# Kernel optimization log

Hardware: AMD Instinct MI355X
Metric: run time of the kernel (lower is better)

## Reference

```python
import jax, jax.numpy as jnp
import numpy as np

DIM = 240
LATENT = 8
TRIALITY = 3
NUM_EXPERTS = 8
TOP_K = 2
DEPTH = 8
B, S = 8, 2048
EPS = 1e-5  # torch LayerNorm default


def get_e8_roots():
    roots = []
    for i in range(8):
        for j in range(i + 1, 8):
            for s0, s1 in [(1, 1), (1, -1), (-1, 1), (-1, -1)]:
                v = np.zeros(8, dtype=np.float32)
                v[i] = s0
                v[j] = s1
                roots.append(v)
                roots.append(-v)
    for signs in range(1 << 8):
        v = np.array([1 if signs & (1 << k) else -1 for k in range(8)], dtype=np.float32) * 0.5
        if bin(signs).count('1') % 2 == 0:
            roots.append(v)
            roots.append(-v)
    roots = np.stack(roots[:240]).astype(np.float32)
    return roots / np.linalg.norm(roots, axis=-1, keepdims=True)


def setup_inputs() -> dict:
    key = jax.random.key(0)
    ks = jax.random.split(key, 6)
    x = jax.random.normal(ks[0], (B, S, DIM), dtype=jnp.float32)
    roots = jnp.asarray(get_e8_roots())  # [240, 8] buffer
    proj_W = jax.random.normal(ks[1], (LATENT, DIM // TRIALITY), dtype=jnp.float32) * 0.02
    gate_W = jax.random.normal(ks[2], (DEPTH, DIM, NUM_EXPERTS), dtype=jnp.float32) * 0.02
    gate_b = jnp.zeros((DEPTH, NUM_EXPERTS), dtype=jnp.float32)
    expert_W = jax.random.normal(ks[3], (DEPTH, NUM_EXPERTS, DIM, DIM), dtype=jnp.float32) * 0.02
    expert_b = jnp.zeros((DEPTH, NUM_EXPERTS, DIM), dtype=jnp.float32)
    ln_gamma = jnp.ones((DIM,), dtype=jnp.float32)
    ln_beta = jnp.zeros((DIM,), dtype=jnp.float32)
    head_W = jax.random.normal(ks[4], (DIM, 1), dtype=jnp.float32) * 0.02
    head_b = jnp.zeros((1,), dtype=jnp.float32)
    return dict(x=x, step=10, roots=roots, proj_W=proj_W, gate_W=gate_W, gate_b=gate_b,
                expert_W=expert_W, expert_b=expert_b, ln_gamma=ln_gamma, ln_beta=ln_beta,
                head_W=head_W, head_b=head_b)


def _layernorm(h, g, b):
    m = h.mean(-1, keepdims=True)
    v = ((h - m) ** 2).mean(-1, keepdims=True)
    return (h - m) / jnp.sqrt(v + EPS) * g + b


def _cycle_block(x, step, roots, proj_W):
    s = x.shape[1]
    pos_emb = roots[jnp.arange(s) % 240]          # [S, 8]
    low_dim = pos_emb @ proj_W                     # [S, 80]
    emb = jnp.tile(low_dim, (1, TRIALITY))         # [S, 240]
    pump = 0.8 * jnp.sin(step * 0.006 * 2.0 * jnp.pi)
    x1 = x * (jnp.cos(emb) + pump)
    x2 = jnp.roll(x1, 1, axis=-1) * jnp.sin(emb)
    x3 = jnp.roll(x2, 1, axis=-1) * jnp.cos(emb)
    return (x1 + x2 + x3) / TRIALITY


def _moe_layer(h, gW, gb, eW, eb):
    gate = jax.nn.softmax(h @ gW + gb, axis=-1)               # [b,s,E]
    tw, ti = jax.lax.top_k(gate, TOP_K)                       # [b,s,k]
    tw = tw / tw.sum(-1, keepdims=True)
    # per-expert combine weight (0 for non-selected experts)
    combine = (jax.nn.one_hot(ti, NUM_EXPERTS, dtype=h.dtype) * tw[..., None]).sum(-2)  # [b,s,E]
    eout = jnp.einsum('bsd,edf->bsef', h, eW) + eb            # [b,s,E,f]
    return jnp.einsum('bsef,bse->bsf', eout, combine)


def reference(x, step, roots, proj_W, gate_W, gate_b, expert_W, expert_b,
              ln_gamma, ln_beta, head_W, head_b):
    h = _cycle_block(x, step, roots, proj_W)

    def body(h, p):
        gW, gb, eW, eb = p
        h = _moe_layer(h, gW, gb, eW, eb)
        h = h + _layernorm(h, ln_gamma, ln_beta)  # norm of layer output, as in source
        return h, None

    h, _ = jax.lax.scan(body, h, (gate_W, gate_b, expert_W, expert_b))
    pooled = h.mean(axis=1)                       # [b, dim]
    return jax.nn.sigmoid(pooled @ head_W + head_b)
```

## Files before the change

kernel.cpp:

```cpp
#include <hip/hip_runtime.h>
#include <math.h>

#define DIM 240
#define NE 8
#define DEPTH 8
#define BB 8
#define SS 2048
#define NTOK (BB * SS)
#define TWO_PI 6.28318530717958647692f
#define NPAIR 28
#define PCAP 4096
#define ASS 264
#define MT 64
#define CMT 32
#define LTILES (PCAP / MT)

typedef __attribute__((ext_vector_type(8))) short s16x8;
typedef __attribute__((ext_vector_type(4))) float f32x4;

#define ALIGN256(x) (((x) + 255) & ~((size_t)255))
static constexpr size_t HBSZ   = (size_t)NPAIR * PCAP * DIM * 2;
static constexpr size_t ENTSZ  = (size_t)NPAIR * PCAP * 4;
static constexpr size_t OFF_HB0    = 0;
static constexpr size_t OFF_HB1    = ALIGN256(OFF_HB0 + HBSZ);
static constexpr size_t OFF_ET0    = ALIGN256(OFF_HB1 + HBSZ);
static constexpr size_t OFF_ET1    = ALIGN256(OFF_ET0 + ENTSZ);
static constexpr size_t OFF_WL0    = ALIGN256(OFF_ET1 + ENTSZ);
static constexpr size_t OFF_WL1    = ALIGN256(OFF_WL0 + ENTSZ);
static constexpr size_t OFF_WH0    = ALIGN256(OFF_WL1 + ENTSZ);
static constexpr size_t OFF_WH1    = ALIGN256(OFF_WH0 + ENTSZ);
static constexpr size_t OFF_CUR    = ALIGN256(OFF_WH1 + ENTSZ);
static constexpr size_t OFF_OUTACC = ALIGN256(OFF_CUR + DEPTH*NPAIR*4);
static constexpr size_t WPACK_PER_E = 8 * 16 * 64 * 8;
static constexpr size_t OFF_WPACK  = ALIGN256(OFF_OUTACC + 8*4);
static constexpr size_t OFF_GWP    = ALIGN256(OFF_WPACK + 64*WPACK_PER_E*2);

__device__ inline short f2bf(float x) {
    unsigned u = __builtin_bit_cast(unsigned, x);
    u += 0x7fffu + ((u >> 16) & 1u);
    return (short)(u >> 16);
}
__device__ inline float bf2f(short s) {
    unsigned u = ((unsigned)(unsigned short)s) << 16;
    return __builtin_bit_cast(float, u);
}
__device__ inline int pidx(int a, int b) {
    return a*7 - ((a*(a-1)) >> 1) + (b - a - 1);
}

struct GAux {
    float lg[MT][NE];
    int   le[MT], lli[MT], lpos[MT];
    float lwl[MT], lwh[MT];
    int   lcnt[NPAIR], lbase[NPAIR];
};

__device__ void pair_gate(const short* hsb, GAux* X, const int* stok,
                          int NT, int ntok, const short* gWp,
                          int* __restrict__ cursor_out,
                          int* __restrict__ entT, float* __restrict__ wlo,
                          float* __restrict__ whi, short* __restrict__ hbo, int tid) {
    int wave = tid >> 6, lane = tid & 63;
    if (tid < NPAIR) X->lcnt[tid] = 0;
    if (wave * 16 < NT) {
        f32x4 g = (f32x4){0.f, 0.f, 0.f, 0.f};
        const short* ar = hsb + (wave*16 + (lane & 15))*ASS + (lane >> 4)*8;
#pragma unroll
        for (int ks = 0; ks < 8; ++ks) {
            s16x8 af = *(const s16x8*)(ar + ks*32);
            s16x8 bf = *(const s16x8*)(gWp + ks*512 + lane*8);
            g = __builtin_amdgcn_mfma_f32_16x16x32_bf16(af, bf, g, 0, 0, 0);
        }
        int e = lane & 15;
        if (e < NE) {
            int r0 = wave*16 + (lane >> 4)*4;
            X->lg[r0+0][e] = g[0];
            X->lg[r0+1][e] = g[1];
            X->lg[r0+2][e] = g[2];
            X->lg[r0+3][e] = g[3];
        }
    }
    __syncthreads();
    if (tid < ntok) {
        int i0 = 0; float v0 = X->lg[tid][0];
#pragma unroll
        for (int k = 1; k < NE; ++k) { float v = X->lg[tid][k]; if (v > v0) { v0 = v; i0 = k; } }
        int i1 = -1; float v1 = -1e30f;
#pragma unroll
        for (int k = 0; k < NE; ++k) { float v = X->lg[tid][k]; if (k != i0 && v > v1) { v1 = v; i1 = k; } }
        float e1 = expf(v1 - v0);
        float w0 = 1.0f / (1.0f + e1);
        float w1 = e1 / (1.0f + e1);
        int a = min(i0, i1), b = max(i0, i1);
        X->lwl[tid] = (i0 < i1) ? w0 : w1;
        X->lwh[tid] = (i0 < i1) ? w1 : w0;
        int c = pidx(a, b);
        int li = atomicAdd(&X->lcnt[c], 1);
        X->le[tid] = c; X->lli[tid] = li;
    }
    __syncthreads();
    if (tid < NPAIR && X->lcnt[tid] > 0)
        X->lbase[tid] = atomicAdd(&cursor_out[tid], X->lcnt[tid]);
    __syncthreads();
    if (tid < ntok) {
        int c = X->le[tid];
        int pos = c*PCAP + X->lbase[c] + X->lli[tid];
        X->lpos[tid] = pos;
        entT[pos] = stok[tid];
        wlo[pos]  = X->lwl[tid];
        whi[pos]  = X->lwh[tid];
    }
    __syncthreads();
    for (int idx = tid; idx < ntok*30; idx += 256) {
        int row = idx / 30, c8 = idx - row*30;
        *(s16x8*)(hbo + (size_t)X->lpos[row]*DIM + c8*8) =
            *(const s16x8*)(hsb + row*ASS + c8*8);
    }
}


__global__ __launch_bounds__(256) void k_cycle(
        const float* __restrict__ x, const int* __restrict__ step,
        const float* __restrict__ roots, const float* __restrict__ projW,
        const float* __restrict__ gateW, const float* __restrict__ eW,
        int* __restrict__ cursor0, int* __restrict__ entT0,
        float* __restrict__ wlo0, float* __restrict__ whi0, short* __restrict__ hb0,
        short* __restrict__ gwp, short* __restrict__ wp) {
    int bid = blockIdx.x, tid = threadIdx.x;
    int wave = tid >> 6, lane = tid & 63;

    if (bid >= 2560) {
        int L = bid - 2560;
        for (int ks = wave; ks < 8; ks += 4) {
            int e = lane & 15;
            int d0 = ks*32 + (lane >> 4)*8;
            short v[8];
#pragma unroll
            for (int j = 0; j < 8; ++j) {
                int d = d0 + j;
                v[j] = (e < NE && d < DIM) ? f2bf(gateW[(size_t)L*DIM*NE + d*NE + e]) : (short)0;
            }
            *(s16x8*)(gwp + ((size_t)L*8 + ks)*512 + lane*8) = *(s16x8*)v;
        }
        return;
    }
    if (bid >= 512) {
        int unit = (bid - 512)*4 + wave;
        int eg = unit >> 7;
        int rem = unit & 127;
        int ks = rem >> 4, tile = rem & 15;
        int f  = tile*16 + (lane & 15);
        int d0 = ks*32 + (lane >> 4)*8;
        const float* W = eW + (size_t)eg*DIM*DIM;
        short v[8];
#pragma unroll
        for (int j = 0; j < 8; ++j) {
            int d = d0 + j;
            v[j] = (d < DIM && f < DIM) ? f2bf(W[(size_t)d*DIM + f]) : (short)0;
        }
        *(s16x8*)(wp + (((size_t)eg*8 + ks)*16 + tile)*512 + lane*8) = *(s16x8*)v;
        return;
    }

    __shared__ short hsb[CMT*ASS];
    __shared__ GAux X;
    __shared__ int stok[CMT];
    __shared__ short gwl[8*512];
    __shared__ float pjw[8*80];

    int tok0 = bid * CMT;
    if (tid < CMT) stok[tid] = tok0 + tid;
    for (int idx = tid; idx < CMT*12; idx += 256) {
        int row = idx / 12, c = 240 + (idx - row*12)*2;
        *(int*)(hsb + row*ASS + c) = 0;
    }
    for (int i = tid; i < 8*80; i += 256) pjw[i] = projW[i];
    for (int u = tid; u < 512; u += 256) {
        int ks = u >> 6, l64 = u & 63;
        int e = l64 & 15, d0 = ks*32 + (l64 >> 4)*8;
        short v[8];
#pragma unroll
        for (int j = 0; j < 8; ++j) {
            int d = d0 + j;
            v[j] = (e < NE && d < DIM) ? f2bf(gateW[d*NE + e]) : (short)0;
        }
        *(s16x8*)(gwl + u*8) = *(s16x8*)v;
    }
    __syncthreads();

    float pump = 0.8f * sinf((float)step[0] * 0.006f * TWO_PI);
    if (lane < 60) {
        int d0 = lane * 4;
        for (int jt = 0; jt < 8; ++jt) {
            int lt = wave * 8 + jt;
            int tok = tok0 + lt;
            int smr = (tok & (SS-1)) % 240;
            const float* xr = x + (size_t)tok * DIM;
            float r8[8];
#pragma unroll
            for (int r = 0; r < 8; ++r) r8[r] = roots[smr*8 + r];
            float xv[6], c6[6], s6[6];
#pragma unroll
            for (int j = 0; j < 6; ++j) {
                int d = d0 - 2 + j; if (d < 0) d += DIM;
                int jm = d % 80;
                float acc = 0.f;
#pragma unroll
                for (int r = 0; r < 8; ++r) acc += r8[r] * pjw[r*80 + jm];
                c6[j] = cosf(acc); s6[j] = sinf(acc);
                xv[j] = xr[d];
            }
            float x1[6];
#pragma unroll
            for (int j = 0; j < 6; ++j) x1[j] = xv[j] * (c6[j] + pump);
            short ob[4];
#pragma unroll
            for (int k = 0; k < 4; ++k)
                ob[k] = f2bf((x1[k+2] + x1[k+1]*s6[k+2] + x1[k]*s6[k+1]*c6[k+2]) * (1.0f/3.0f));
            *(short4*)(hsb + lt*ASS + d0) = *(short4*)ob;
        }
    }
    __syncthreads();
    pair_gate(hsb, &X, stok, CMT, CMT, gwl, cursor0, entT0, wlo0, whi0, hb0, tid);
}

__global__ __launch_bounds__(256, 2) void k_layer(
        const short* __restrict__ hb_in, const int* __restrict__ entT_in,
        const float* __restrict__ wlo_in, const float* __restrict__ whi_in,
        short* __restrict__ hb_out, int* __restrict__ entT_out,
        float* __restrict__ wlo_out, float* __restrict__ whi_out,
        const short* __restrict__ wpack, const float* __restrict__ eb,
        const float* __restrict__ gamma, const float* __restrict__ beta,
        const short* __restrict__ gwp_next,
        const int* __restrict__ cursor_in, int* __restrict__ cursor_out,
        const float* __restrict__ headW, float* __restrict__ out_acc,
        int l, int do_gate) {
    __shared__ short As[MT*ASS];
    __shared__ GAux X;
    __shared__ float swl[MT], swh[MT];
    __shared__ int stok[MT];
    __shared__ float part[4][MT][2];
    __shared__ float mrs[MT][2];
    __shared__ float pool[BB];

    int p = blockIdx.x, tile = blockIdx.y;
    int cnt = cursor_in[p];
    int t0 = tile * MT;
    if (t0 >= cnt) return;
    int ntok = min(MT, cnt - t0);
    int tid = threadIdx.x, wave = tid >> 6, lane = tid & 63;
    int a = 0, rem = p;
    while (rem >= 7 - a) { rem -= 7 - a; ++a; }
    int b = a + 1 + rem;
    size_t base = (size_t)p * PCAP + t0;

    if (tid < MT) {
        if (tid < ntok) { stok[tid] = entT_in[base+tid]; swl[tid] = wlo_in[base+tid]; swh[tid] = whi_in[base+tid]; }
        else            { stok[tid] = 0; swl[tid] = 0.f; swh[tid] = 0.f; }
    }
    if (tid < BB) pool[tid] = 0.f;
#pragma unroll
    for (int it = 0; it < 8; ++it) {
        int idx = tid + it * 256;
        int row = idx >> 5, c8 = idx & 31;
        s16x8 z = (s16x8){0,0,0,0,0,0,0,0};
        if (c8 < 30 && row < ntok)
            z = *(const s16x8*)(hb_in + (base + row)*DIM + c8*8);
        *(s16x8*)(As + row*ASS + ((c8 < 30) ? c8*8 : (240 + (c8-30)*8))) = z;
    }
    __syncthreads();

    f32x4 accA[4][4], accB[4][4];
#pragma unroll
    for (int m = 0; m < 4; ++m)
#pragma unroll
        for (int n = 0; n < 4; ++n) { accA[m][n] = (f32x4){0,0,0,0}; accB[m][n] = (f32x4){0,0,0,0}; }

    const short* ab = As + (lane & 15)*ASS + (lane >> 4)*8;
    const short* wA = wpack + ((size_t)(l*NE + a))*WPACK_PER_E + (size_t)wave*4*512 + lane*8;
    const short* wB = wpack + ((size_t)(l*NE + b))*WPACK_PER_E + (size_t)wave*4*512 + lane*8;

    for (int ks = 0; ks < 8; ++ks) {
        s16x8 a0 = *(const s16x8*)(ab + ks*32 + 0*16*ASS);
        s16x8 a1 = *(const s16x8*)(ab + ks*32 + 1*16*ASS);
        s16x8 a2 = *(const s16x8*)(ab + ks*32 + 2*16*ASS);
        s16x8 a3 = *(const s16x8*)(ab + ks*32 + 3*16*ASS);
#pragma unroll
        for (int n = 0; n < 4; ++n) {
            s16x8 bA = *(const s16x8*)(wA + ((size_t)ks*16 + n)*512);
            s16x8 bB = *(const s16x8*)(wB + ((size_t)ks*16 + n)*512);
            accA[0][n] = __builtin_amdgcn_mfma_f32_16x16x32_bf16(a0, bA, accA[0][n], 0, 0, 0);
            accA[1][n] = __builtin_amdgcn_mfma_f32_16x16x32_bf16(a1, bA, accA[1][n], 0, 0, 0);
            accA[2][n] = __builtin_amdgcn_mfma_f32_16x16x32_bf16(a2, bA, accA[2][n], 0, 0, 0);
            accA[3][n] = __builtin_amdgcn_mfma_f32_16x16x32_bf16(a3, bA, accA[3][n], 0, 0, 0);
            accB[0][n] = __builtin_amdgcn_mfma_f32_16x16x32_bf16(a0, bB, accB[0][n], 0, 0, 0);
            accB[1][n] = __builtin_amdgcn_mfma_f32_16x16x32_bf16(a1, bB, accB[1][n], 0, 0, 0);
            accB[2][n] = __builtin_amdgcn_mfma_f32_16x16x32_bf16(a2, bB, accB[2][n], 0, 0, 0);
            accB[3][n] = __builtin_amdgcn_mfma_f32_16x16x32_bf16(a3, bB, accB[3][n], 0, 0, 0);
        }
    }
    __syncthreads();

    const float* ebA = eb + ((size_t)(l*NE + a))*DIM;
    const float* ebB = eb + ((size_t)(l*NE + b))*DIM;
    float bA[4], bBv[4], gg[4], bt[4]; int colv[4];
#pragma unroll
    for (int n = 0; n < 4; ++n) {
        int col = wave*64 + n*16 + (lane & 15);
        bool valid = (col < DIM);
        colv[n] = valid ? col : -1;
        bA[n]  = valid ? ebA[col]   : 0.f;
        bBv[n] = valid ? ebB[col]   : 0.f;
        gg[n]  = valid ? gamma[col] : 0.f;
        bt[n]  = valid ? beta[col]  : 0.f;
    }

#pragma unroll
    for (int m = 0; m < 4; ++m) {
#pragma unroll
        for (int r = 0; r < 4; ++r) {
            int row = m*16 + ((lane >> 4) << 2) + r;
            float wa = swl[row], wb = swh[row];
            float s = 0.f, q = 0.f;
#pragma unroll
            for (int n = 0; n < 4; ++n) {
                float y = (colv[n] >= 0)
                        ? wa*(accA[m][n][r] + bA[n]) + wb*(accB[m][n][r] + bBv[n]) : 0.f;
                s += y; q += y*y;
            }
#pragma unroll
            for (int o = 1; o <= 8; o <<= 1) {
                s += __shfl_xor(s, o, 64);
                q += __shfl_xor(q, o, 64);
            }
            if ((lane & 15) == 0) { part[wave][row][0] = s; part[wave][row][1] = q; }
        }
    }
    __syncthreads();
    if (tid < MT) {
        float s = part[0][tid][0] + part[1][tid][0] + part[2][tid][0] + part[3][tid][0];
        float q = part[0][tid][1] + part[1][tid][1] + part[2][tid][1] + part[3][tid][1];
        float mean = s * (1.0f/DIM);
        float var = q * (1.0f/DIM) - mean*mean;
        mrs[tid][0] = mean;
        mrs[tid][1] = rsqrtf(var + 1e-5f);
    }
    __syncthreads();
    for (int idx = tid; idx < MT*12; idx += 256) {
        int row = idx / 12, c = 240 + (idx - row*12)*2;
        *(int*)(As + row*ASS + c) = 0;
    }
#pragma unroll
    for (int m = 0; m < 4; ++m) {
#pragma unroll
        for (int r = 0; r < 4; ++r) {
            int row = m*16 + ((lane >> 4) << 2) + r;
            float wa = swl[row], wb = swh[row];
            float mean = mrs[row][0], rs = mrs[row][1];
#pragma unroll
            for (int n = 0; n < 4; ++n) {
                if (colv[n] >= 0) {
                    float y = wa*(accA[m][n][r] + bA[n]) + wb*(accB[m][n][r] + bBv[n]);
                    As[row*ASS + colv[n]] = f2bf(y + (y - mean)*rs*gg[n] + bt[n]);
                }
            }
        }
    }
    __syncthreads();

    if (do_gate) {
        pair_gate(As, &X, stok, MT, ntok, gwp_next,
                  cursor_out, entT_out, wlo_out, whi_out, hb_out, tid);
    } else {
        float hwv[4];
#pragma unroll
        for (int jj = 0; jj < 4; ++jj) {
            int d = lane + 64*jj;
            hwv[jj] = (d < DIM) ? headW[d] : 0.f;
        }
        for (int j = 0; j < 16; ++j) {
            int row = wave*16 + j;
            if (row >= ntok) continue;
            float ph = 0.f;
#pragma unroll
            for (int jj = 0; jj < 4; ++jj) {
                int d = lane + 64*jj;
                if (d < DIM) ph += bf2f(As[row*ASS + d]) * hwv[jj];
            }
#pragma unroll
            for (int o = 32; o > 0; o >>= 1) ph += __shfl_xor(ph, o, 64);
            if (lane == 0) atomicAdd(&pool[stok[row] / SS], ph);
        }
        __syncthreads();
        if (tid < BB) atomicAdd(&out_acc[tid], pool[tid]);
    }
}

__global__ void k_final(const float* __restrict__ out_acc, const float* __restrict__ headb,
                        float* __restrict__ out) {
    int b = threadIdx.x;
    if (b < BB) {
        float z = out_acc[b] * (1.0f/SS) + headb[0];
        out[b] = 1.0f / (1.0f + expf(-z));
    }
}

extern "C" void kernel_launch(void* const* d_in, const int* in_sizes, int n_in,
                              void* d_out, int out_size, void* d_ws, size_t ws_size,
                              hipStream_t stream) {
    (void)in_sizes; (void)n_in; (void)out_size; (void)ws_size;
    const float* x     = (const float*)d_in[0];
    const int*   step  = (const int*)  d_in[1];
    const float* roots = (const float*)d_in[2];
    const float* projW = (const float*)d_in[3];
    const float* gateW = (const float*)d_in[4];
    const float* eW    = (const float*)d_in[6];
    const float* eb    = (const float*)d_in[7];
    const float* gamma = (const float*)d_in[8];
    const float* beta  = (const float*)d_in[9];
    const float* headW = (const float*)d_in[10];
    const float* headb = (const float*)d_in[11];
    float* out = (float*)d_out;

    char* w = (char*)d_ws;
    short* hb[2]   = { (short*)(w + OFF_HB0), (short*)(w + OFF_HB1) };
    int*   et[2]   = { (int*)  (w + OFF_ET0), (int*)  (w + OFF_ET1) };
    float* wl[2]   = { (float*)(w + OFF_WL0), (float*)(w + OFF_WL1) };
    float* wh[2]   = { (float*)(w + OFF_WH0), (float*)(w + OFF_WH1) };
    int*   cursor  = (int*)  (w + OFF_CUR);
    float* out_acc = (float*)(w + OFF_OUTACC);
    short* wpack   = (short*)(w + OFF_WPACK);
    short* gwp     = (short*)(w + OFF_GWP);

    hipMemsetAsync(w + OFF_CUR, 0, (OFF_OUTACC - OFF_CUR) + BB*sizeof(float), stream);

    k_cycle<<<2568, 256, 0, stream>>>(x, step, roots, projW, gateW, eW,
                                      cursor, et[0], wl[0], wh[0], hb[0], gwp, wpack);

    for (int l = 0; l < DEPTH; ++l) {
        int in = l & 1, outp = in ^ 1;
        int do_gate = (l < DEPTH - 1);
        const short* gwn = gwp + (size_t)(do_gate ? (l+1) : 0) * 8 * 512;
        int* cur_out = cursor + (do_gate ? (l+1) : 0) * NPAIR;
        k_layer<<<dim3(NPAIR, LTILES), 256, 0, stream>>>(
            hb[in], et[in], wl[in], wh[in],
            hb[outp], et[outp], wl[outp], wh[outp],
            wpack, eb, gamma, beta, gwn,
            cursor + l*NPAIR, cur_out, headW, out_acc, l, do_gate);
    }

    k_final<<<1, 64, 0, stream>>>(out_acc, headb, out);
}
```

Baseline: 319.7 us.

## Fuse all MoE layers into one persistent per-token-tile kernel

Replaces the per-layer pair-bucketed dispatch, with its global scatter of hidden states and atomic cursors, by one kernel in which each 512-thread block keeps 64 tokens resident in LDS across all 8 layers. Inside each layer the block gates, groups its tokens by expert locally, runs the MFMA expert GEMMs on gathered rows and accumulates the weighted outputs into an fp32 LDS buffer before LayerNorm. This removes 8 launches and the global round-trips of activations. In exchange it uses roughly 120 KB of LDS, so only one block fits per CU. Expert tiles are often partly filled, which wastes MFMA work, and expert weights are re-read from L2 by every block.

New measurement: 518.0 us. 62.1% more time.

```diff
diff --git a/kernel.cpp b/kernel.cpp
--- a/kernel.cpp
+++ b/kernel.cpp
@@ -8,32 +8,34 @@
 #define SS 2048
 #define NTOK (BB * SS)
 #define TWO_PI 6.28318530717958647692f
-#define NPAIR 28
-#define PCAP 4096
 #define ASS 264
-#define MT 64
-#define CMT 32
-#define LTILES (PCAP / MT)
+#define YSS 244
+#define TPB 512
+#define ROWS 64
+#define NBLK (NTOK / ROWS)
+#define NT_TILES 15
 
 typedef __attribute__((ext_vector_type(8))) short s16x8;
 typedef __attribute__((ext_vector_type(4))) float f32x4;
 
-#define ALIGN256(x) (((x) + 255) & ~((size_t)255))
-static constexpr size_t HBSZ   = (size_t)NPAIR * PCAP * DIM * 2;
-static constexpr size_t ENTSZ  = (size_t)NPAIR * PCAP * 4;
-static constexpr size_t OFF_HB0    = 0;
-static constexpr size_t OFF_HB1    = ALIGN256(OFF_HB0 + HBSZ);
-static constexpr size_t OFF_ET0    = ALIGN256(OFF_HB1 + HBSZ);
-static constexpr size_t OFF_ET1    = ALIGN256(OFF_ET0 + ENTSZ);
-static constexpr size_t OFF_WL0    = ALIGN256(OFF_ET1 + ENTSZ);
-static constexpr size_t OFF_WL1    = ALIGN256(OFF_WL0 + ENTSZ);
-static constexpr size_t OFF_WH0    = ALIGN256(OFF_WL1 + ENTSZ);
-static constexpr size_t OFF_WH1    = ALIGN256(OFF_WH0 + ENTSZ);
-static constexpr size_t OFF_CUR    = ALIGN256(OFF_WH1 + ENTSZ);
-static constexpr size_t OFF_OUTACC = ALIGN256(OFF_CUR + DEPTH*NPAIR*4);
 static constexpr size_t WPACK_PER_E = 8 * 16 * 64 * 8;
-static constexpr size_t OFF_WPACK  = ALIGN256(OFF_OUTACC + 8*4);
-static constexpr size_t OFF_GWP    = ALIGN256(OFF_WPACK + 64*WPACK_PER_E*2);
+static constexpr size_t OFF_OUTACC = 0;
+static constexpr size_t OFF_WPACK  = 256;
+static constexpr size_t OFF_GWP    = OFF_WPACK + 64 * WPACK_PER_E * 2;
+
+#define L_HSB   0
+#define L_Y     33792
+#define L_GWL   96256
+#define L_EBL   104448
+#define L_GML   112128
+#define L_BTL   113088
+#define L_LG    114048
+#define L_RL    116096
+#define L_RW    117120
+#define L_CNT   119168
+#define L_POOL  119232
+#define L_PJW   119264
+#define SMEM_SZ 121824
 
 __device__ inline short f2bf(float x) {
     unsigned u = __builtin_bit_cast(unsigned, x);
@@ -44,93 +46,15 @@
     unsigned u = ((unsigned)(unsigned short)s) << 16;
     return __builtin_bit_cast(float, u);
 }
-__device__ inline int pidx(int a, int b) {
-    return a*7 - ((a*(a-1)) >> 1) + (b - a - 1);
-}
-
-struct GAux {
-    float lg[MT][NE];
-    int   le[MT], lli[MT], lpos[MT];
-    float lwl[MT], lwh[MT];
-    int   lcnt[NPAIR], lbase[NPAIR];
-};
-
-__device__ void pair_gate(const short* hsb, GAux* X, const int* stok,
-                          int NT, int ntok, const short* gWp,
-                          int* __restrict__ cursor_out,
-                          int* __restrict__ entT, float* __restrict__ wlo,
-                          float* __restrict__ whi, short* __restrict__ hbo, int tid) {
-    int wave = tid >> 6, lane = tid & 63;
-    if (tid < NPAIR) X->lcnt[tid] = 0;
-    if (wave * 16 < NT) {
-        f32x4 g = (f32x4){0.f, 0.f, 0.f, 0.f};
-        const short* ar = hsb + (wave*16 + (lane & 15))*ASS + (lane >> 4)*8;
-#pragma unroll
-        for (int ks = 0; ks < 8; ++ks) {
-            s16x8 af = *(const s16x8*)(ar + ks*32);
-            s16x8 bf = *(const s16x8*)(gWp + ks*512 + lane*8);
-            g = __builtin_amdgcn_mfma_f32_16x16x32_bf16(af, bf, g, 0, 0, 0);
-        }
-        int e = lane & 15;
-        if (e < NE) {
-            int r0 = wave*16 + (lane >> 4)*4;
-            X->lg[r0+0][e] = g[0];
-            X->lg[r0+1][e] = g[1];
-            X->lg[r0+2][e] = g[2];
-            X->lg[r0+3][e] = g[3];
-        }
-    }
-    __syncthreads();
-    if (tid < ntok) {
-        int i0 = 0; float v0 = X->lg[tid][0];
-#pragma unroll
-        for (int k = 1; k < NE; ++k) { float v = X->lg[tid][k]; if (v > v0) { v0 = v; i0 = k; } }
-        int i1 = -1; float v1 = -1e30f;
-#pragma unroll
-        for (int k = 0; k < NE; ++k) { float v = X->lg[tid][k]; if (k != i0 && v > v1) { v1 = v; i1 = k; } }
-        float e1 = expf(v1 - v0);
-        float w0 = 1.0f / (1.0f + e1);
-        float w1 = e1 / (1.0f + e1);
-        int a = min(i0, i1), b = max(i0, i1);
-        X->lwl[tid] = (i0 < i1) ? w0 : w1;
-        X->lwh[tid] = (i0 < i1) ? w1 : w0;
-        int c = pidx(a, b);
-        int li = atomicAdd(&X->lcnt[c], 1);
-        X->le[tid] = c; X->lli[tid] = li;
-    }
-    __syncthreads();
-    if (tid < NPAIR && X->lcnt[tid] > 0)
-        X->lbase[tid] = atomicAdd(&cursor_out[tid], X->lcnt[tid]);
-    __syncthreads();
-    if (tid < ntok) {
-        int c = X->le[tid];
-        int pos = c*PCAP + X->lbase[c] + X->lli[tid];
-        X->lpos[tid] = pos;
-        entT[pos] = stok[tid];
-        wlo[pos]  = X->lwl[tid];
-        whi[pos]  = X->lwh[tid];
-    }
-    __syncthreads();
-    for (int idx = tid; idx < ntok*30; idx += 256) {
-        int row = idx / 30, c8 = idx - row*30;
-        *(s16x8*)(hbo + (size_t)X->lpos[row]*DIM + c8*8) =
-            *(const s16x8*)(hsb + row*ASS + c8*8);
-    }
-}
-
-
-__global__ __launch_bounds__(256) void k_cycle(
-        const float* __restrict__ x, const int* __restrict__ step,
-        const float* __restrict__ roots, const float* __restrict__ projW,
-        const float* __restrict__ gateW, const float* __restrict__ eW,
-        int* __restrict__ cursor0, int* __restrict__ entT0,
-        float* __restrict__ wlo0, float* __restrict__ whi0, short* __restrict__ hb0,
-        short* __restrict__ gwp, short* __restrict__ wp) {
+
+__global__ __launch_bounds__(256) void k_pack(const float* __restrict__ gateW,
+                                              const float* __restrict__ eW,
+                                              short* __restrict__ gwp,
+                                              short* __restrict__ wp) {
     int bid = blockIdx.x, tid = threadIdx.x;
     int wave = tid >> 6, lane = tid & 63;
-
-    if (bid >= 2560) {
-        int L = bid - 2560;
+    if (bid >= 2048) {
+        int L = bid - 2048;
         for (int ks = wave; ks < 8; ks += 4) {
             int e = lane & 15;
             int d0 = ks*32 + (lane >> 4)*8;
@@ -144,47 +68,51 @@
         }
         return;
     }
-    if (bid >= 512) {
-        int unit = (bid - 512)*4 + wave;
-        int eg = unit >> 7;
-        int rem = unit & 127;
-        int ks = rem >> 4, tile = rem & 15;
-        int f  = tile*16 + (lane & 15);
-        int d0 = ks*32 + (lane >> 4)*8;
-        const float* W = eW + (size_t)eg*DIM*DIM;
-        short v[8];
-#pragma unroll
-        for (int j = 0; j < 8; ++j) {
-            int d = d0 + j;
-            v[j] = (d < DIM && f < DIM) ? f2bf(W[(size_t)d*DIM + f]) : (short)0;
-        }
-        *(s16x8*)(wp + (((size_t)eg*8 + ks)*16 + tile)*512 + lane*8) = *(s16x8*)v;
-        return;
-    }
-
-    __shared__ short hsb[CMT*ASS];
-    __shared__ GAux X;
-    __shared__ int stok[CMT];
-    __shared__ short gwl[8*512];
-    __shared__ float pjw[8*80];
-
-    int tok0 = bid * CMT;
-    if (tid < CMT) stok[tid] = tok0 + tid;
-    for (int idx = tid; idx < CMT*12; idx += 256) {
+    int unit = bid*4 + wave;
+    int eg = unit >> 7;
+    int rem = unit & 127;
+    int ks = rem >> 4, tile = rem & 15;
+    int f  = tile*16 + (lane & 15);
+    int d0 = ks*32 + (lane >> 4)*8;
+    const float* W = eW + (size_t)eg*DIM*DIM;
+    short v[8];
+#pragma unroll
+    for (int j = 0; j < 8; ++j) {
+        int d = d0 + j;
+        v[j] = (d < DIM && f < DIM) ? f2bf(W[(size_t)d*DIM + f]) : (short)0;
+    }
+    *(s16x8*)(wp + (((size_t)eg*8 + ks)*16 + tile)*512 + lane*8) = *(s16x8*)v;
+}
+
+__global__ __launch_bounds__(TPB, 1) void k_main(
+        const float* __restrict__ x, const int* __restrict__ step,
+        const float* __restrict__ roots, const float* __restrict__ projW,
+        const short* __restrict__ wpack, const short* __restrict__ gwp,
+        const float* __restrict__ eb, const float* __restrict__ gamma,
+        const float* __restrict__ beta, const float* __restrict__ headW,
+        float* __restrict__ out_acc) {
+    extern __shared__ char smem[];
+    short* hsb = (short*)(smem + L_HSB);
+    float* y   = (float*)(smem + L_Y);
+    short* gwl = (short*)(smem + L_GWL);
+    float* ebl = (float*)(smem + L_EBL);
+    float* gml = (float*)(smem + L_GML);
+    float* btl = (float*)(smem + L_BTL);
+    float* lg  = (float*)(smem + L_LG);
+    short* rl  = (short*)(smem + L_RL);
+    float* rw  = (float*)(smem + L_RW);
+    int*   cnt = (int*)  (smem + L_CNT);
+    float* pool= (float*)(smem + L_POOL);
+    float* pjw = (float*)(smem + L_PJW);
+
+    const int tid = threadIdx.x, wave = tid >> 6, lane = tid & 63;
+    const int tok0 = blockIdx.x * ROWS;
+
+    for (int i = tid; i < 8*80; i += TPB) pjw[i] = projW[i];
+    for (int i = tid; i < DIM; i += TPB) { gml[i] = gamma[i]; btl[i] = beta[i]; }
+    for (int idx = tid; idx < ROWS*12; idx += TPB) {
         int row = idx / 12, c = 240 + (idx - row*12)*2;
         *(int*)(hsb + row*ASS + c) = 0;
-    }
-    for (int i = tid; i < 8*80; i += 256) pjw[i] = projW[i];
-    for (int u = tid; u < 512; u += 256) {
-        int ks = u >> 6, l64 = u & 63;
-        int e = l64 & 15, d0 = ks*32 + (l64 >> 4)*8;
-        short v[8];
-#pragma unroll
-        for (int j = 0; j < 8; ++j) {
-            int d = d0 + j;
-            v[j] = (e < NE && d < DIM) ? f2bf(gateW[d*NE + e]) : (short)0;
-        }
-        *(s16x8*)(gwl + u*8) = *(s16x8*)v;
     }
     __syncthreads();
 
@@ -221,179 +149,148 @@
         }
     }
     __syncthreads();
-    pair_gate(hsb, &X, stok, CMT, CMT, gwl, cursor0, entT0, wlo0, whi0, hb0, tid);
-}
-
-__global__ __launch_bounds__(256, 2) void k_layer(
-        const short* __restrict__ hb_in, const int* __restrict__ entT_in,
-        const float* __restrict__ wlo_in, const float* __restrict__ whi_in,
-        short* __restrict__ hb_out, int* __restrict__ entT_out,
-        float* __restrict__ wlo_out, float* __restrict__ whi_out,
-        const short* __restrict__ wpack, const float* __restrict__ eb,
-        const float* __restrict__ gamma, const float* __restrict__ beta,
-        const short* __restrict__ gwp_next,
-        const int* __restrict__ cursor_in, int* __restrict__ cursor_out,
-        const float* __restrict__ headW, float* __restrict__ out_acc,
-        int l, int do_gate) {
-    __shared__ short As[MT*ASS];
-    __shared__ GAux X;
-    __shared__ float swl[MT], swh[MT];
-    __shared__ int stok[MT];
-    __shared__ float part[4][MT][2];
-    __shared__ float mrs[MT][2];
-    __shared__ float pool[BB];
-
-    int p = blockIdx.x, tile = blockIdx.y;
-    int cnt = cursor_in[p];
-    int t0 = tile * MT;
-    if (t0 >= cnt) return;
-    int ntok = min(MT, cnt - t0);
-    int tid = threadIdx.x, wave = tid >> 6, lane = tid & 63;
-    int a = 0, rem = p;
-    while (rem >= 7 - a) { rem -= 7 - a; ++a; }
-    int b = a + 1 + rem;
-    size_t base = (size_t)p * PCAP + t0;
-
-    if (tid < MT) {
-        if (tid < ntok) { stok[tid] = entT_in[base+tid]; swl[tid] = wlo_in[base+tid]; swh[tid] = whi_in[base+tid]; }
-        else            { stok[tid] = 0; swl[tid] = 0.f; swh[tid] = 0.f; }
-    }
-    if (tid < BB) pool[tid] = 0.f;
-#pragma unroll
-    for (int it = 0; it < 8; ++it) {
-        int idx = tid + it * 256;
-        int row = idx >> 5, c8 = idx & 31;
-        s16x8 z = (s16x8){0,0,0,0,0,0,0,0};
-        if (c8 < 30 && row < ntok)
-            z = *(const s16x8*)(hb_in + (base + row)*DIM + c8*8);
-        *(s16x8*)(As + row*ASS + ((c8 < 30) ? c8*8 : (240 + (c8-30)*8))) = z;
-    }
+
+    for (int l = 0; l < DEPTH; ++l) {
+        if (tid < 512) ((s16x8*)gwl)[tid] = ((const s16x8*)(gwp + (size_t)l*4096))[tid];
+        for (int i = tid; i < NE*DIM; i += TPB) ebl[i] = eb[(size_t)l*NE*DIM + i];
+        for (int idx = tid; idx < ROWS*DIM; idx += TPB)
+            y[(idx/DIM)*YSS + (idx % DIM)] = 0.f;
+        if (tid < NE) cnt[tid] = 0;
+        rl[tid & 511] = 0;
+        __syncthreads();
+
+        if (wave < 4) {
+            f32x4 g = (f32x4){0.f, 0.f, 0.f, 0.f};
+            const short* ar = hsb + (wave*16 + (lane & 15))*ASS + (lane >> 4)*8;
+#pragma unroll
+            for (int ks = 0; ks < 8; ++ks) {
+                s16x8 af = *(const s16x8*)(ar + ks*32);
+                s16x8 bf = *(const s16x8*)(gwl + ks*512 + lane*8);
+                g = __builtin_amdgcn_mfma_f32_16x16x32_bf16(af, bf, g, 0, 0, 0);
+            }
+            int e = lane & 15;
+            if (e < NE) {
+                int r0 = wave*16 + (lane >> 4)*4;
+                lg[(r0+0)*NE + e] = g[0];
+                lg[(r0+1)*NE + e] = g[1];
+                lg[(r0+2)*NE + e] = g[2];
+                lg[(r0+3)*NE + e] = g[3];
+            }
+        }
+        __syncthreads();
+
+        if (tid < ROWS) {
+            int i0 = 0; float v0 = lg[tid*NE];
+#pragma unroll
+            for (int k = 1; k < NE; ++k) { float v = lg[tid*NE + k]; if (v > v0) { v0 = v; i0 = k; } }
+            int i1 = -1; float v1 = -1e30f;
+#pragma unroll
+            for (int k = 0; k < NE; ++k) { float v = lg[tid*NE + k]; if (k != i0 && v > v1) { v1 = v; i1 = k; } }
+            float e1 = expf(v1 - v0);
+            float w0 = 1.0f / (1.0f + e1);
+            float w1 = e1 / (1.0f + e1);
+            int a, b; float wa, wb;
+            if (i0 < i1) { a = i0; b = i1; wa = w0; wb = w1; }
+            else         { a = i1; b = i0; wa = w1; wb = w0; }
+            int li = atomicAdd(&cnt[a], 1); rl[a*64 + li] = (short)tid; rw[a*64 + li] = wa;
+            int lj = atomicAdd(&cnt[b], 1); rl[b*64 + lj] = (short)tid; rw[b*64 + lj] = wb;
+        }
+        __syncthreads();
+
+        const short* wpl = wpack + (size_t)l*NE*WPACK_PER_E + lane*8;
+        for (int e = 0; e < NE; ++e) {
+            int ce = cnt[e];
+            if (ce == 0) continue;
+            int me = (ce + 15) >> 4;
+            const short* wpe = wpl + (size_t)e*WPACK_PER_E;
+            int r0i = rl[e*64 +  0 + (lane & 15)];
+            int r1i = (me > 1) ? rl[e*64 + 16 + (lane & 15)] : 0;
+            int r2i = (me > 2) ? rl[e*64 + 32 + (lane & 15)] : 0;
+            int r3i = (me > 3) ? rl[e*64 + 48 + (lane & 15)] : 0;
+#pragma unroll
+            for (int t = 0; t < 2; ++t) {
+                int nt = wave + t*8;
+                if (nt >= NT_TILES) continue;
+                f32x4 a0 = (f32x4){0,0,0,0}, a1 = a0, a2 = a0, a3 = a0;
+                for (int ks = 0; ks < 8; ++ks) {
+                    s16x8 bf = *(const s16x8*)(wpe + ((size_t)ks*16 + nt)*512);
+                    int ko = (lane >> 4)*8 + ks*32;
+                    s16x8 f0 = *(const s16x8*)(hsb + r0i*ASS + ko);
+                    a0 = __builtin_amdgcn_mfma_f32_16x16x32_bf16(f0, bf, a0, 0, 0, 0);
+                    if (me > 1) {
+                        s16x8 f1 = *(const s16x8*)(hsb + r1i*ASS + ko);
+                        a1 = __builtin_amdgcn_mfma_f32_16x16x32_bf16(f1, bf, a1, 0, 0, 0);
+                    }
+                    if (me > 2) {
+                        s16x8 f2 = *(const s16x8*)(hsb + r2i*ASS + ko);
+                        a2 = __builtin_amdgcn_mfma_f32_16x16x32_bf16(f2, bf, a2, 0, 0, 0);
+                    }
+                    if (me > 3) {
+                        s16x8 f3 = *(const s16x8*)(hsb + r3i*ASS + ko);
+                        a3 = __builtin_amdgcn_mfma_f32_16x16x32_bf16(f3, bf, a3, 0, 0, 0);
+                    }
+                }
+                int colb = nt*16 + (lane & 15);
+                float ebc = ebl[e*DIM + colb];
+#pragma unroll
+                for (int m = 0; m < 4; ++m) {
+                    if (m >= me) break;
+                    f32x4 am = (m == 0) ? a0 : (m == 1) ? a1 : (m == 2) ? a2 : a3;
+#pragma unroll
+                    for (int r = 0; r < 4; ++r) {
+                        int pos = m*16 + (lane >> 4)*4 + r;
+                        if (pos < ce) {
+                            int row = rl[e*64 + pos];
+                            float w = rw[e*64 + pos];
+                            y[row*YSS + colb] += w * (am[r] + ebc);
+                        }
+                    }
+                }
+            }
+        }
+        __syncthreads();
+
+        {
+            int row = tid >> 3, k = tid & 7;
+            const float* yr = y + row*YSS + k*30;
+            float s = 0.f, q = 0.f;
+#pragma unroll
+            for (int j = 0; j < 30; ++j) { float v = yr[j]; s += v; q += v*v; }
+            s += __shfl_xor(s, 1, 64); q += __shfl_xor(q, 1, 64);
+            s += __shfl_xor(s, 2, 64); q += __shfl_xor(q, 2, 64);
+            s += __shfl_xor(s, 4, 64); q += __shfl_xor(q, 4, 64);
+            float mean = s * (1.0f/DIM);
+            float var  = q * (1.0f/DIM) - mean*mean;
+            float rs   = rsqrtf(var + 1e-5f);
+            short* hr = hsb + row*ASS + k*30;
+#pragma unroll
+            for (int j = 0; j < 30; ++j) {
+                int col = k*30 + j;
+                float v = yr[j];
+                hr[j] = f2bf(v + (v - mean)*rs*gml[col] + btl[col]);
+            }
+        }
+        __syncthreads();
+    }
+
+    float* hwl = pjw;
+    for (int i = tid; i < DIM; i += TPB) hwl[i] = headW[i];
+    if (tid == 0) pool[0] = 0.f;
     __syncthreads();
-
-    f32x4 accA[4][4], accB[4][4];
-#pragma unroll
-    for (int m = 0; m < 4; ++m)
-#pragma unroll
-        for (int n = 0; n < 4; ++n) { accA[m][n] = (f32x4){0,0,0,0}; accB[m][n] = (f32x4){0,0,0,0}; }
-
-    const short* ab = As + (lane & 15)*ASS + (lane >> 4)*8;
-    const short* wA = wpack + ((size_t)(l*NE + a))*WPACK_PER_E + (size_t)wave*4*512 + lane*8;
-    const short* wB = wpack + ((size_t)(l*NE + b))*WPACK_PER_E + (size_t)wave*4*512 + lane*8;
-
-    for (int ks = 0; ks < 8; ++ks) {
-        s16x8 a0 = *(const s16x8*)(ab + ks*32 + 0*16*ASS);
-        s16x8 a1 = *(const s16x8*)(ab + ks*32 + 1*16*ASS);
-        s16x8 a2 = *(const s16x8*)(ab + ks*32 + 2*16*ASS);
-        s16x8 a3 = *(const s16x8*)(ab + ks*32 + 3*16*ASS);
-#pragma unroll
-        for (int n = 0; n < 4; ++n) {
-            s16x8 bA = *(const s16x8*)(wA + ((size_t)ks*16 + n)*512);
-            s16x8 bB = *(const s16x8*)(wB + ((size_t)ks*16 + n)*512);
-            accA[0][n] = __builtin_amdgcn_mfma_f32_16x16x32_bf16(a0, bA, accA[0][n], 0, 0, 0);
-            accA[1][n] = __builtin_amdgcn_mfma_f32_16x16x32_bf16(a1, bA, accA[1][n], 0, 0, 0);
-            accA[2][n] = __builtin_amdgcn_mfma_f32_16x16x32_bf16(a2, bA, accA[2][n], 0, 0, 0);
-            accA[3][n] = __builtin_amdgcn_mfma_f32_16x16x32_bf16(a3, bA, accA[3][n], 0, 0, 0);
-            accB[0][n] = __builtin_amdgcn_mfma_f32_16x16x32_bf16(a0, bB, accB[0][n], 0, 0, 0);
-            accB[1][n] = __builtin_amdgcn_mfma_f32_16x16x32_bf16(a1, bB, accB[1][n], 0, 0, 0);
-            accB[2][n] = __builtin_amdgcn_mfma_f32_16x16x32_bf16(a2, bB, accB[2][n], 0, 0, 0);
-            accB[3][n] = __builtin_amdgcn_mfma_f32_16x16x32_bf16(a3, bB, accB[3][n], 0, 0, 0);
-        }
+    {
+        int row = tid >> 3, k = tid & 7;
+        const short* hr = hsb + row*ASS + k*30;
+        const float* hw = hwl + k*30;
+        float ph = 0.f;
+#pragma unroll
+        for (int j = 0; j < 30; ++j) ph += bf2f(hr[j]) * hw[j];
+        ph += __shfl_xor(ph, 1, 64);
+        ph += __shfl_xor(ph, 2, 64);
+        ph += __shfl_xor(ph, 4, 64);
+        if (k == 0) atomicAdd(&pool[0], ph);
     }
     __syncthreads();
-
-    const float* ebA = eb + ((size_t)(l*NE + a))*DIM;
-    const float* ebB = eb + ((size_t)(l*NE + b))*DIM;
-    float bA[4], bBv[4], gg[4], bt[4]; int colv[4];
-#pragma unroll
-    for (int n = 0; n < 4; ++n) {
-        int col = wave*64 + n*16 + (lane & 15);
-        bool valid = (col < DIM);
-        colv[n] = valid ? col : -1;
-        bA[n]  = valid ? ebA[col]   : 0.f;
-        bBv[n] = valid ? ebB[col]   : 0.f;
-        gg[n]  = valid ? gamma[col] : 0.f;
-        bt[n]  = valid ? beta[col]  : 0.f;
-    }
-
-#pragma unroll
-    for (int m = 0; m < 4; ++m) {
-#pragma unroll
-        for (int r = 0; r < 4; ++r) {
-            int row = m*16 + ((lane >> 4) << 2) + r;
-            float wa = swl[row], wb = swh[row];
-            float s = 0.f, q = 0.f;
-#pragma unroll
-            for (int n = 0; n < 4; ++n) {
-                float y = (colv[n] >= 0)
-                        ? wa*(accA[m][n][r] + bA[n]) + wb*(accB[m][n][r] + bBv[n]) : 0.f;
-                s += y; q += y*y;
-            }
-#pragma unroll
-            for (int o = 1; o <= 8; o <<= 1) {
-                s += __shfl_xor(s, o, 64);
-                q += __shfl_xor(q, o, 64);
-            }
-            if ((lane & 15) == 0) { part[wave][row][0] = s; part[wave][row][1] = q; }
-        }
-    }
-    __syncthreads();
-    if (tid < MT) {
-        float s = part[0][tid][0] + part[1][tid][0] + part[2][tid][0] + part[3][tid][0];
-        float q = part[0][tid][1] + part[1][tid][1] + part[2][tid][1] + part[3][tid][1];
-        float mean = s * (1.0f/DIM);
-        float var = q * (1.0f/DIM) - mean*mean;
-        mrs[tid][0] = mean;
-        mrs[tid][1] = rsqrtf(var + 1e-5f);
-    }
-    __syncthreads();
-    for (int idx = tid; idx < MT*12; idx += 256) {
-        int row = idx / 12, c = 240 + (idx - row*12)*2;
-        *(int*)(As + row*ASS + c) = 0;
-    }
-#pragma unroll
-    for (int m = 0; m < 4; ++m) {
-#pragma unroll
-        for (int r = 0; r < 4; ++r) {
-            int row = m*16 + ((lane >> 4) << 2) + r;
-            float wa = swl[row], wb = swh[row];
-            float mean = mrs[row][0], rs = mrs[row][1];
-#pragma unroll
-            for (int n = 0; n < 4; ++n) {
-                if (colv[n] >= 0) {
-                    float y = wa*(accA[m][n][r] + bA[n]) + wb*(accB[m][n][r] + bBv[n]);
-                    As[row*ASS + colv[n]] = f2bf(y + (y - mean)*rs*gg[n] + bt[n]);
-                }
-            }
-        }
-    }
-    __syncthreads();
-
-    if (do_gate) {
-        pair_gate(As, &X, stok, MT, ntok, gwp_next,
-                  cursor_out, entT_out, wlo_out, whi_out, hb_out, tid);
-    } else {
-        float hwv[4];
-#pragma unroll
-        for (int jj = 0; jj < 4; ++jj) {
-            int d = lane + 64*jj;
-            hwv[jj] = (d < DIM) ? headW[d] : 0.f;
-        }
-        for (int j = 0; j < 16; ++j) {
-            int row = wave*16 + j;
-            if (row >= ntok) continue;
-            float ph = 0.f;
-#pragma unroll
-            for (int jj = 0; jj < 4; ++jj) {
-                int d = lane + 64*jj;
-                if (d < DIM) ph += bf2f(As[row*ASS + d]) * hwv[jj];
-            }
-#pragma unroll
-            for (int o = 32; o > 0; o >>= 1) ph += __shfl_xor(ph, o, 64);
-            if (lane == 0) atomicAdd(&pool[stok[row] / SS], ph);
-        }
-        __syncthreads();
-        if (tid < BB) atomicAdd(&out_acc[tid], pool[tid]);
-    }
+    if (tid == 0) atomicAdd(&out_acc[tok0 / SS], pool[0]);
 }
 
 __global__ void k_final(const float* __restrict__ out_acc, const float* __restrict__ headb,
@@ -423,31 +320,20 @@
     float* out = (float*)d_out;
 
     char* w = (char*)d_ws;
-    short* hb[2]   = { (short*)(w + OFF_HB0), (short*)(w + OFF_HB1) };
-    int*   et[2]   = { (int*)  (w + OFF_ET0), (int*)  (w + OFF_ET1) };
-    float* wl[2]   = { (float*)(w + OFF_WL0), (float*)(w + OFF_WL1) };
-    float* wh[2]   = { (float*)(w + OFF_WH0), (float*)(w + OFF_WH1) };
-    int*   cursor  = (int*)  (w + OFF_CUR);
     float* out_acc = (float*)(w + OFF_OUTACC);
     short* wpack   = (short*)(w + OFF_WPACK);
     short* gwp     = (short*)(w + OFF_GWP);
 
-    hipMemsetAsync(w + OFF_CUR, 0, (OFF_OUTACC - OFF_CUR) + BB*sizeof(float), stream);
-
-    k_cycle<<<2568, 256, 0, stream>>>(x, step, roots, projW, gateW, eW,
-                                      cursor, et[0], wl[0], wh[0], hb[0], gwp, wpack);
-
-    for (int l = 0; l < DEPTH; ++l) {
-        int in = l & 1, outp = in ^ 1;
-        int do_gate = (l < DEPTH - 1);
-        const short* gwn = gwp + (size_t)(do_gate ? (l+1) : 0) * 8 * 512;
-        int* cur_out = cursor + (do_gate ? (l+1) : 0) * NPAIR;
-        k_layer<<<dim3(NPAIR, LTILES), 256, 0, stream>>>(
-            hb[in], et[in], wl[in], wh[in],
-            hb[outp], et[outp], wl[outp], wh[outp],
-            wpack, eb, gamma, beta, gwn,
-            cursor + l*NPAIR, cur_out, headW, out_acc, l, do_gate);
-    }
-
+    static bool inited = false;
+    if (!inited) {
+        hipFuncSetAttribute(reinterpret_cast<const void*>(k_main),
+                            hipFuncAttributeMaxDynamicSharedMemorySize, SMEM_SZ);
+        inited = true;
+    }
+
+    hipMemsetAsync(w + OFF_OUTACC, 0, BB*sizeof(float), stream);
+    k_pack<<<2056, 256, 0, stream>>>(gateW, eW, gwp, wpack);
+    k_main<<<NBLK, TPB, SMEM_SZ, stream>>>(x, step, roots, projW, wpack, gwp,
+                                           eb, gamma, beta, headW, out_acc);
     k_final<<<1, 64, 0, stream>>>(out_acc, headb, out);
 }
```
